# Performance work log

Measured on AMD Instinct MI355X. Metric: run time of the kernel, lower is better.

The kernel has to match this reference:

```python
import jax, jax.numpy as jnp
import numpy as np

# Each of the 16 soft logic gates g(a,b) is affine in {1, a, b, a*b}.
# COEFF[g] = [k0, ka, kb, kab] so that gate_g = k0 + ka*a + kb*b + kab*a*b.
COEFF = np.array([
    [0,  0,  0,  0],   # 0: False
    [0,  0,  0,  1],   # 1: a AND b
    [0,  1,  0, -1],   # 2: a AND NOT b
    [0,  1,  0,  0],   # 3: a
    [0,  0,  1, -1],   # 4: NOT a AND b
    [0,  0,  1,  0],   # 5: b
    [0,  1,  1, -2],   # 6: XOR
    [0,  1,  1, -1],   # 7: OR
    [1, -1, -1,  1],   # 8: NOR
    [1, -1, -1,  2],   # 9: XNOR
    [1,  0, -1,  0],   # 10: NOT b
    [1,  0, -1,  1],   # 11: a OR NOT b
    [1, -1,  0,  0],   # 12: NOT a
    [1, -1,  0,  1],   # 13: NOT a OR b
    [1,  0,  0, -1],   # 14: NAND
    [1,  0,  0,  0],   # 15: True
], dtype=np.float32)

BATCH, IN_DIM, OUT_DIM, N_GATES = 2048, 16384, 16384, 16


def setup_inputs() -> dict:
    key = jax.random.key(0)
    k1, k2, k3, k4 = jax.random.split(key, 4)
    x = jax.random.uniform(k1, (BATCH, IN_DIM), dtype=jnp.float32)
    weights = jax.random.normal(k2, (OUT_DIM, N_GATES), dtype=jnp.float32)
    idx_a = jax.random.randint(k3, (OUT_DIM,), 0, IN_DIM, dtype=jnp.int64)
    idx_b = jax.random.randint(k4, (OUT_DIM,), 0, IN_DIM, dtype=jnp.int64)
    return {"x": x, "weights": weights, "idx_a": idx_a, "idx_b": idx_b}


def reference(x, weights, idx_a, idx_b):
    # Training-mode forward: softmax mixture over the 16 logic gates.
    nw = jax.nn.softmax(weights, axis=-1)            # [out, 16]
    W = nw @ jnp.asarray(COEFF, dtype=x.dtype)       # [out, 4] effective affine coeffs
    a = x[:, idx_a]                                  # [batch, out]
    b = x[:, idx_b]                                  # [batch, out]
    ab = a * b
    # r = sum_g nw[:,g] * gate_g(a,b) == W0 + Wa*a + Wb*b + Wab*ab
    return W[:, 0] + W[:, 1] * a + W[:, 2] * b + W[:, 3] * ab
```

## Files before the change

kernel.cpp:

```cpp
#include <hip/hip_runtime.h>

#define BATCH   2048
#define IN_DIM  16384
#define OUT_DIM 16384
#define NGATES  16

typedef float    f32x4 __attribute__((ext_vector_type(4)));
typedef _Float16 f16x4 __attribute__((ext_vector_type(4)));
typedef _Float16 f16x8 __attribute__((ext_vector_type(8)));

__constant__ float c_coeff[NGATES][4] = {
    {0, 0, 0, 0},  {0, 0, 0, 1},  {0, 1, 0, -1}, {0, 1, 0, 0},
    {0, 0, 1, -1}, {0, 0, 1, 0},  {0, 1, 1, -2}, {0, 1, 1, -1},
    {1, -1, -1, 1},{1, -1, -1, 2},{1, 0, -1, 0}, {1, 0, -1, 1},
    {1, -1, 0, 0}, {1, -1, 0, 1}, {1, 0, 0, -1}, {1, 0, 0, 0}
};

__global__ __launch_bounds__(256) void prep_kernel(
    const float* __restrict__ weights,
    const int*   __restrict__ idx_a,
    const int*   __restrict__ idx_b,
    f16x4*       __restrict__ Wh,
    unsigned*    __restrict__ Ipk)
{
    int j = blockIdx.x * blockDim.x + threadIdx.x;
    if (j >= OUT_DIM) return;

    const float4* wrow = reinterpret_cast<const float4*>(weights + (size_t)j * NGATES);
    float v[NGATES];
    float4 q0 = wrow[0], q1 = wrow[1], q2 = wrow[2], q3 = wrow[3];
    v[0]=q0.x; v[1]=q0.y; v[2]=q0.z; v[3]=q0.w;
    v[4]=q1.x; v[5]=q1.y; v[6]=q1.z; v[7]=q1.w;
    v[8]=q2.x; v[9]=q2.y; v[10]=q2.z; v[11]=q2.w;
    v[12]=q3.x; v[13]=q3.y; v[14]=q3.z; v[15]=q3.w;

    float m = v[0];
#pragma unroll
    for (int g = 1; g < NGATES; ++g) m = fmaxf(m, v[g]);
    float s = 0.f;
#pragma unroll
    for (int g = 0; g < NGATES; ++g) { v[g] = expf(v[g] - m); s += v[g]; }
    float inv = 1.0f / s;

    float c0 = 0.f, c1 = 0.f, c2 = 0.f, c3 = 0.f;
#pragma unroll
    for (int g = 0; g < NGATES; ++g) {
        c0 += v[g] * c_coeff[g][0];
        c1 += v[g] * c_coeff[g][1];
        c2 += v[g] * c_coeff[g][2];
        c3 += v[g] * c_coeff[g][3];
    }
    f16x4 h;
    h.x = (_Float16)(c0 * inv); h.y = (_Float16)(c1 * inv);
    h.z = (_Float16)(c2 * inv); h.w = (_Float16)(c3 * inv);
    Wh[j] = h;
    Ipk[j] = (unsigned)idx_a[j] | ((unsigned)idx_b[j] << 16);
}

__global__ __launch_bounds__(1024, 4) void logic_row_kernel(
    const float* __restrict__ x,
    const f16x8* __restrict__ Wh8,
    const uint4* __restrict__ Ipk4,
    float*       __restrict__ out)
{
    __shared__ float row[IN_DIM];
    const int tid = threadIdx.x;
    const int i   = blockIdx.x;

    const f32x4* xr = reinterpret_cast<const f32x4*>(x + (size_t)i * IN_DIM);
    f32x4* rr = reinterpret_cast<f32x4*>(row);
#pragma unroll
    for (int k = 0; k < 4; ++k) rr[tid + k * 1024] = xr[tid + k * 1024];

    uint4 q[4];
    f16x8 w[8];
#pragma unroll
    for (int k = 0; k < 4; ++k) {
        q[k]       = Ipk4[tid + k * 1024];
        w[2*k]     = Wh8[(size_t)(tid + k * 1024) * 2];
        w[2*k + 1] = Wh8[(size_t)(tid + k * 1024) * 2 + 1];
    }

    __syncthreads();

    float av[16], bv[16];
#pragma unroll
    for (int k = 0; k < 4; ++k) {
        av[4*k+0] = row[q[k].x & 0xFFFFu];  bv[4*k+0] = row[q[k].x >> 16];
        av[4*k+1] = row[q[k].y & 0xFFFFu];  bv[4*k+1] = row[q[k].y >> 16];
        av[4*k+2] = row[q[k].z & 0xFFFFu];  bv[4*k+2] = row[q[k].z >> 16];
        av[4*k+3] = row[q[k].w & 0xFFFFu];  bv[4*k+3] = row[q[k].w >> 16];
    }

    f32x4* o4 = reinterpret_cast<f32x4*>(out + (size_t)i * OUT_DIM);
#pragma unroll
    for (int k = 0; k < 4; ++k) {
        f16x8 wa = w[2*k], wb = w[2*k + 1];
        float a0 = av[4*k+0], b0 = bv[4*k+0];
        float a1 = av[4*k+1], b1 = bv[4*k+1];
        float a2 = av[4*k+2], b2 = bv[4*k+2];
        float a3 = av[4*k+3], b3 = bv[4*k+3];

        f32x4 res;
        res.x = (float)wa[0] + (float)wa[1] * a0 + (float)wa[2] * b0 + (float)wa[3] * (a0 * b0);
        res.y = (float)wa[4] + (float)wa[5] * a1 + (float)wa[6] * b1 + (float)wa[7] * (a1 * b1);
        res.z = (float)wb[0] + (float)wb[1] * a2 + (float)wb[2] * b2 + (float)wb[3] * (a2 * b2);
        res.w = (float)wb[4] + (float)wb[5] * a3 + (float)wb[6] * b3 + (float)wb[7] * (a3 * b3);
        __builtin_nontemporal_store(res, &o4[tid + k * 1024]);
    }
}

extern "C" void kernel_launch(void* const* d_in, const int* in_sizes, int n_in,
                              void* d_out, int out_size, void* d_ws, size_t ws_size,
                              hipStream_t stream) {
    const float* x       = (const float*)d_in[0];
    const float* weights = (const float*)d_in[1];
    const int*   idx_a   = (const int*)d_in[2];
    const int*   idx_b   = (const int*)d_in[3];
    float* out = (float*)d_out;

    f16x4*    Wh  = (f16x4*)d_ws;
    unsigned* Ipk = (unsigned*)((char*)d_ws + (size_t)OUT_DIM * sizeof(f16x4));

    prep_kernel<<<(OUT_DIM + 255) / 256, 256, 0, stream>>>(weights, idx_a, idx_b, Wh, Ipk);
    logic_row_kernel<<<BATCH, 1024, 0, stream>>>(x, (const f16x8*)Wh, (const uint4*)Ipk, out);
}
```

Baseline: 56.26 us.

## Stage input row as fp16 in LDS, halve block size, software-pipeline gathers

Converts each input row to fp16 while staging it in shared memory, halving LDS use to 32 KB per block so more blocks can be resident. The block size drops to 512 threads and each thread loops over 8 output groups, prefetching the next index/weight vectors during the current gather. This trades fp32 precision of x (uniform in [0,1]) for fp16, adding rounding error, and each thread now runs a serial loop with more iterations.

After: 49.14 us, median of 2. -12.7%, faster.

```diff
diff --git a/kernel.cpp b/kernel.cpp
--- a/kernel.cpp
+++ b/kernel.cpp
@@ -57,56 +57,57 @@
     Ipk[j] = (unsigned)idx_a[j] | ((unsigned)idx_b[j] << 16);
 }
 
-__global__ __launch_bounds__(1024, 4) void logic_row_kernel(
+__global__ __launch_bounds__(512, 8) void logic_row_kernel(
     const float* __restrict__ x,
     const f16x8* __restrict__ Wh8,
     const uint4* __restrict__ Ipk4,
     float*       __restrict__ out)
 {
-    __shared__ float row[IN_DIM];
+    __shared__ _Float16 rowh[IN_DIM];
     const int tid = threadIdx.x;
     const int i   = blockIdx.x;
 
-    const f32x4* xr = reinterpret_cast<const f32x4*>(x + (size_t)i * IN_DIM);
-    f32x4* rr = reinterpret_cast<f32x4*>(row);
+    const f32x4* xr  = reinterpret_cast<const f32x4*>(x + (size_t)i * IN_DIM);
+    f16x4*       rhw = reinterpret_cast<f16x4*>(rowh);
 #pragma unroll
-    for (int k = 0; k < 4; ++k) rr[tid + k * 1024] = xr[tid + k * 1024];
+    for (int k = 0; k < IN_DIM / 4 / 512; ++k) {
+        f32x4 v = xr[tid + k * 512];
+        f16x4 h;
+        h.x = (_Float16)v.x; h.y = (_Float16)v.y;
+        h.z = (_Float16)v.z; h.w = (_Float16)v.w;
+        rhw[tid + k * 512] = h;
+    }
 
-    uint4 q[4];
-    f16x8 w[8];
-#pragma unroll
-    for (int k = 0; k < 4; ++k) {
-        q[k]       = Ipk4[tid + k * 1024];
-        w[2*k]     = Wh8[(size_t)(tid + k * 1024) * 2];
-        w[2*k + 1] = Wh8[(size_t)(tid + k * 1024) * 2 + 1];
-    }
+    uint4 qc = Ipk4[tid];
+    f16x8 wa = Wh8[(size_t)tid * 2];
+    f16x8 wb = Wh8[(size_t)tid * 2 + 1];
 
     __syncthreads();
 
-    float av[16], bv[16];
-#pragma unroll
-    for (int k = 0; k < 4; ++k) {
-        av[4*k+0] = row[q[k].x & 0xFFFFu];  bv[4*k+0] = row[q[k].x >> 16];
-        av[4*k+1] = row[q[k].y & 0xFFFFu];  bv[4*k+1] = row[q[k].y >> 16];
-        av[4*k+2] = row[q[k].z & 0xFFFFu];  bv[4*k+2] = row[q[k].z >> 16];
-        av[4*k+3] = row[q[k].w & 0xFFFFu];  bv[4*k+3] = row[q[k].w >> 16];
-    }
+    f32x4* o4 = reinterpret_cast<f32x4*>(out + (size_t)i * OUT_DIM);
 
-    f32x4* o4 = reinterpret_cast<f32x4*>(out + (size_t)i * OUT_DIM);
-#pragma unroll
-    for (int k = 0; k < 4; ++k) {
-        f16x8 wa = w[2*k], wb = w[2*k + 1];
-        float a0 = av[4*k+0], b0 = bv[4*k+0];
-        float a1 = av[4*k+1], b1 = bv[4*k+1];
-        float a2 = av[4*k+2], b2 = bv[4*k+2];
-        float a3 = av[4*k+3], b3 = bv[4*k+3];
+    for (int k = 0; k < OUT_DIM / 4 / 512; ++k) {
+        uint4 qn;  f16x8 wan, wbn;
+        if (k + 1 < OUT_DIM / 4 / 512) {
+            const int j4n = tid + (k + 1) * 512;
+            qn  = Ipk4[j4n];
+            wan = Wh8[(size_t)j4n * 2];
+            wbn = Wh8[(size_t)j4n * 2 + 1];
+        }
+
+        float a0 = (float)rowh[qc.x & 0xFFFFu], b0 = (float)rowh[qc.x >> 16];
+        float a1 = (float)rowh[qc.y & 0xFFFFu], b1 = (float)rowh[qc.y >> 16];
+        float a2 = (float)rowh[qc.z & 0xFFFFu], b2 = (float)rowh[qc.z >> 16];
+        float a3 = (float)rowh[qc.w & 0xFFFFu], b3 = (float)rowh[qc.w >> 16];
 
         f32x4 res;
         res.x = (float)wa[0] + (float)wa[1] * a0 + (float)wa[2] * b0 + (float)wa[3] * (a0 * b0);
         res.y = (float)wa[4] + (float)wa[5] * a1 + (float)wa[6] * b1 + (float)wa[7] * (a1 * b1);
         res.z = (float)wb[0] + (float)wb[1] * a2 + (float)wb[2] * b2 + (float)wb[3] * (a2 * b2);
         res.w = (float)wb[4] + (float)wb[5] * a3 + (float)wb[6] * b3 + (float)wb[7] * (a3 * b3);
-        __builtin_nontemporal_store(res, &o4[tid + k * 1024]);
+        __builtin_nontemporal_store(res, &o4[tid + k * 512]);
+
+        qc = qn; wa = wan; wb = wbn;
     }
 }
 
@@ -123,5 +124,5 @@
     unsigned* Ipk = (unsigned*)((char*)d_ws + (size_t)OUT_DIM * sizeof(f16x4));
 
     prep_kernel<<<(OUT_DIM + 255) / 256, 256, 0, stream>>>(weights, idx_a, idx_b, Wh, Ipk);
-    logic_row_kernel<<<BATCH, 1024, 0, stream>>>(x, (const f16x8*)Wh, (const uint4*)Ipk, out);
+    logic_row_kernel<<<BATCH, 512, 0, stream>>>(x, (const f16x8*)Wh, (const uint4*)Ipk, out);
 }
```
